# Kernel tuning notes

Measured on AMD Instinct MI355X. Metric: run time of the kernel, lower is better.

The kernel has to match this reference:

```python
import jax, jax.numpy as jnp
import numpy as np

NV, B, E, H, LF = 32, 32768, 16, 4, 4
D = E // H
FF = LF * E
EPS = 1e-5


def _gelu(x):
    return jax.nn.gelu(x, approximate=False)


def _ln(x, g, b):
    m = x.mean(-1, keepdims=True)
    v = ((x - m) ** 2).mean(-1, keepdims=True)
    return (x - m) * jax.lax.rsqrt(v + EPS) * g + b


def _mha(q_in, kv_in, wi, bi, wo, bo):
    # torch nn.MultiheadAttention, seq-first layout (S, B, E), eval mode (no dropout)
    wq, wk, wv = jnp.split(wi, 3, axis=0)
    bq, bk, bv = jnp.split(bi, 3)
    Sq, Bn = q_in.shape[0], q_in.shape[1]
    Sk = kv_in.shape[0]
    q = (q_in @ wq.T + bq).reshape(Sq, Bn, H, D)
    k = (kv_in @ wk.T + bk).reshape(Sk, Bn, H, D)
    v = (kv_in @ wv.T + bv).reshape(Sk, Bn, H, D)
    s = jnp.einsum('qbhd,kbhd->bhqk', q, k) / jnp.sqrt(jnp.asarray(D, q.dtype))
    a = jax.nn.softmax(s, axis=-1)
    o = jnp.einsum('bhqk,kbhd->qbhd', a, v).reshape(Sq, Bn, E)
    return o @ wo.T + bo


def setup_inputs() -> dict:
    key = jax.random.key(0)
    ks = iter(jax.random.split(key, 32))
    r = lambda *shape: 0.1 * jax.random.normal(next(ks), shape, dtype=jnp.float32)
    return {
        'x': jax.random.normal(next(ks), (B, NV), dtype=jnp.float32),
        'emb_w1': r(NV, LF), 'emb_b1': r(NV, LF),            # per-feature Linear(1, LF)
        'emb_w2': r(NV, LF, E), 'emb_b2': r(NV, E),          # per-feature Linear(LF, E)
        'ln1_g': jnp.ones((E,), jnp.float32), 'ln1_b': jnp.zeros((E,), jnp.float32),
        'attn_wi': r(3 * E, E), 'attn_bi': r(3 * E),
        'attn_wo': r(E, E), 'attn_bo': r(E),
        'ln2_g': jnp.ones((E,), jnp.float32), 'ln2_b': jnp.zeros((E,), jnp.float32),
        'fc1_w': r(FF, E), 'fc1_b': r(FF),
        'fc2_w': r(E, FF), 'fc2_b': r(E),
        'cls_token': jnp.zeros((E,), jnp.float32),
        'cln1_g': jnp.ones((E,), jnp.float32), 'cln1_b': jnp.zeros((E,), jnp.float32),
        'cattn_wi': r(3 * E, E), 'cattn_bi': r(3 * E),
        'cattn_wo': r(E, E), 'cattn_bo': r(E),
        'cln2_g': jnp.ones((E,), jnp.float32), 'cln2_b': jnp.zeros((E,), jnp.float32),
        'clsfc_w': r(1, E), 'clsfc_b': r(1),
    }


def reference(x, emb_w1, emb_b1, emb_w2, emb_b2, ln1_g, ln1_b,
              attn_wi, attn_bi, attn_wo, attn_bo, ln2_g, ln2_b,
              fc1_w, fc1_b, fc2_w, fc2_b, cls_token,
              cln1_g, cln1_b, cattn_wi, cattn_bi, cattn_wo, cattn_bo,
              cln2_g, cln2_b, clsfc_w, clsfc_b):
    # --- per-feature tokenizer: batched tiny MLPs (vectorized over nvars) ---
    h = _gelu(x[:, :, None] * emb_w1[None] + emb_b1[None])          # (B, NV, LF)
    e = _gelu(jnp.einsum('bvf,vfe->bve', h, emb_w2) + emb_b2[None]) # (B, NV, E)
    t = jnp.transpose(e, (1, 0, 2))                                 # (NV, B, E) seq-first
    # --- encoder block (pre-norm) ---
    res = t
    t = _ln(t, ln1_g, ln1_b)
    t = _mha(t, t, attn_wi, attn_bi, attn_wo, attn_bo) + res
    res = t
    t = _ln(t, ln2_g, ln2_b)
    t = _gelu(t @ fc1_w.T + fc1_b) @ fc2_w.T + fc2_b
    t = t + res
    # --- class-token decoder ---
    cls = jnp.broadcast_to(cls_token, (1, t.shape[1], E))           # (1, B, E)
    u = jnp.concatenate([cls, t], axis=0)                           # (NV+1, B, E)
    un = _ln(u, cln1_g, cln1_b)
    c = _mha(cls, un, cattn_wi, cattn_bi, cattn_wo, cattn_bo) + cls # query is raw cls
    c = _ln(c, cln2_g, cln2_b)
    c = c[0]                                                        # (B, E)
    out = jax.nn.sigmoid(c @ clsfc_w.T + clsfc_b)                   # (B, 1)
    return out
```

## Files before the change

### kernel.cpp

```cpp
#include <hip/hip_runtime.h>
#include <hip/hip_bf16.h>
#include <math.h>

#define NV 32
#define E  16
#define FF 64
#define BATCH 32768

static constexpr float EPS = 1e-5f;

typedef __attribute__((ext_vector_type(8)))  short bf16x8;
typedef __attribute__((ext_vector_type(16))) float f32x16;
typedef __attribute__((ext_vector_type(4)))  unsigned u32x4;

__device__ __forceinline__ short f2bf(float f) {
    __hip_bfloat16 h = __float2bfloat16(f);
    return __builtin_bit_cast(short, h);
}
__device__ __forceinline__ unsigned pack2(float a, float b) {
    return (unsigned)(unsigned short)f2bf(a) | ((unsigned)(unsigned short)f2bf(b) << 16);
}
__device__ __forceinline__ void halfswap(unsigned &a, unsigned &b, int hh) {
    const unsigned ax = (unsigned)__shfl_xor((int)a, 32);
    const unsigned bx = (unsigned)__shfl_xor((int)b, 32);
    const unsigned na = hh ? bx : a;
    const unsigned nb = hh ? b : ax;
    a = na; b = nb;
}
__device__ __forceinline__ int psi(int h, int i) {
    return 4 * h + (i & 3) + 8 * (i >> 2);
}
__device__ __forceinline__ float gelu_fast(float x) {
    const float x2 = x * x;
    const float u  = x * fmaf(x2, 0.07135481627f, 1.5957691216f);
    return x - x * __builtin_amdgcn_rcpf(1.0f + __expf(u));
}
__device__ __forceinline__ bf16x8 pack8(const float* v) {
    bf16x8 r;
#pragma unroll
    for (int i = 0; i < 8; i++) r[i] = f2bf(v[i]);
    return r;
}

__global__ __launch_bounds__(256, 4) void event_classifier_kernel(
    const float* __restrict__ x,
    const float* __restrict__ emb_w1,
    const float* __restrict__ emb_b1,
    const float* __restrict__ emb_w2,
    const float* __restrict__ emb_b2,
    const float* __restrict__ ln1_g, const float* __restrict__ ln1_b,
    const float* __restrict__ attn_wi,
    const float* __restrict__ attn_bi,
    const float* __restrict__ attn_wo,
    const float* __restrict__ attn_bo,
    const float* __restrict__ ln2_g, const float* __restrict__ ln2_b,
    const float* __restrict__ fc1_w,
    const float* __restrict__ fc1_b,
    const float* __restrict__ fc2_w,
    const float* __restrict__ fc2_b,
    const float* __restrict__ cls_token,
    const float* __restrict__ cln1_g, const float* __restrict__ cln1_b,
    const float* __restrict__ cattn_wi,
    const float* __restrict__ cattn_bi,
    const float* __restrict__ cattn_wo,
    const float* __restrict__ cattn_bo,
    const float* __restrict__ cln2_g, const float* __restrict__ cln2_b,
    const float* __restrict__ clsfc_w,
    const float* __restrict__ clsfc_b,
    float* __restrict__ out)
{
    __shared__ alignas(16) unsigned s_frag[13][64][4];
    __shared__ alignas(16) float s_bias[10][32];
    __shared__ alignas(16) unsigned short s_vt[4][4][5][40];
    __shared__ alignas(16) float s_cls[48];

    const int tid = threadIdx.x;
    const int l   = tid & 63;
    const int t   = l & 31;
    const int hh  = l >> 5;
    const int w   = tid >> 6;
    const int b   = blockIdx.x * 4 + w;

    for (int f0 = 0; f0 < 16; f0 += 4) {
        const int f = f0 + w;
        if (f < 13) {
            const float* W;
            switch (f) {
                case 0:  W = attn_wi;        break;
                case 1:  W = attn_wi + 256;  break;
                case 2:  W = attn_wi + 512;  break;
                case 3:  W = attn_wo;        break;
                case 4:  W = fc1_w;          break;
                case 5:  W = fc1_w + 512;    break;
                case 6: case 7: case 8: case 9: W = fc2_w; break;
                case 10: W = cattn_wi + 256; break;
                case 11: W = cattn_wi + 512; break;
                default: W = cattn_wo;       break;
            }
            const int stride = (f >= 6 && f <= 9) ? 64 : 16;
            const int coff   = (f >= 6 && f <= 9) ? (f - 6) * 16 : 0;
            const bool valid = (f == 4 || f == 5) ? true : (t < 16);
            const float scale = (f == 0) ? 0.5f : 1.0f;
            unsigned d0 = 0, d1 = 0, d2 = 0, d3 = 0;
            if (valid) {
                const float* row = W + t * stride + coff;
                d0 = pack2(row[psi(hh, 0)] * scale, row[psi(hh, 1)] * scale);
                d1 = pack2(row[psi(hh, 2)] * scale, row[psi(hh, 3)] * scale);
                d2 = pack2(row[psi(hh, 4)] * scale, row[psi(hh, 5)] * scale);
                d3 = pack2(row[psi(hh, 6)] * scale, row[psi(hh, 7)] * scale);
            }
            s_frag[f][l][0] = d0; s_frag[f][l][1] = d1;
            s_frag[f][l][2] = d2; s_frag[f][l][3] = d3;
        }
    }
    for (int i = tid; i < 10 * 32; i += 256) {
        const int mat = i >> 5, idx = i & 31, h2 = idx >> 4, r = idx & 15;
        const int p8 = psi(h2, r & 7);
        float val = 0.f;
        switch (mat) {
            case 0: if (r < 8) val = attn_bi[p8] * 0.5f; break;
            case 1: if (r < 8) val = attn_bi[16 + p8]; break;
            case 2: if (r < 8) val = attn_bi[32 + p8]; break;
            case 3: if (r < 8) val = attn_bo[p8]; break;
            case 4: val = fc1_b[psi(h2, r)]; break;
            case 5: val = fc1_b[32 + psi(h2, r)]; break;
            case 6: if (r < 8) val = fc2_b[p8]; break;
            case 7: if (r < 8) val = cattn_bi[16 + p8]; break;
            case 8: if (r < 8) val = cattn_bi[32 + p8]; break;
            default: if (r < 8) val = cattn_bo[p8] + cls_token[p8]; break;
        }
        s_bias[mat][idx] = val;
    }
    if (tid < 16) {
        const int jp = tid;
        float cls[E];
        float m = 0.f;
#pragma unroll
        for (int j = 0; j < E; j++) { cls[j] = cls_token[j]; m += cls[j]; }
        m *= (1.0f / E);
        float var = 0.f;
#pragma unroll
        for (int j = 0; j < E; j++) { float d = cls[j] - m; var += d * d; }
        var *= (1.0f / E);
        float r = rsqrtf(var + EPS);
        float un0[E];
#pragma unroll
        for (int j = 0; j < E; j++) un0[j] = (cls[j] - m) * r * cln1_g[j] + cln1_b[j];
        float qq = cattn_bi[jp], kk = cattn_bi[16 + jp], vv2 = cattn_bi[32 + jp];
#pragma unroll
        for (int j = 0; j < E; j++) {
            qq  += cls[j] * cattn_wi[jp * E + j];
            kk  += un0[j] * cattn_wi[(16 + jp) * E + j];
            vv2 += un0[j] * cattn_wi[(32 + jp) * E + j];
        }
        s_cls[jp] = qq * 0.5f; s_cls[16 + jp] = kk; s_cls[32 + jp] = vv2;
    }
    __syncthreads();

#define LD4(p) (*reinterpret_cast<const float4*>(p))
#define FRAG(f) (*reinterpret_cast<const bf16x8*>(&s_frag[f][l][0]))
#define CBIAS8(mat, c) { const float4 lo_ = LD4(&s_bias[mat][hh*16]); \
                         const float4 hi_ = LD4(&s_bias[mat][hh*16+4]); \
                         c[0]=lo_.x; c[1]=lo_.y; c[2]=lo_.z; c[3]=lo_.w; \
                         c[4]=hi_.x; c[5]=hi_.y; c[6]=hi_.z; c[7]=hi_.w; \
                         c[8]=0;c[9]=0;c[10]=0;c[11]=0;c[12]=0;c[13]=0;c[14]=0;c[15]=0; }
#define CBIAS16(mat, c) { const float4 a_ = LD4(&s_bias[mat][hh*16]); \
                          const float4 b_ = LD4(&s_bias[mat][hh*16+4]); \
                          const float4 c_ = LD4(&s_bias[mat][hh*16+8]); \
                          const float4 d_ = LD4(&s_bias[mat][hh*16+12]); \
                          c[0]=a_.x;c[1]=a_.y;c[2]=a_.z;c[3]=a_.w; \
                          c[4]=b_.x;c[5]=b_.y;c[6]=b_.z;c[7]=b_.w; \
                          c[8]=c_.x;c[9]=c_.y;c[10]=c_.z;c[11]=c_.w; \
                          c[12]=d_.x;c[13]=d_.y;c[14]=d_.z;c[15]=d_.w; }

    f32x16 z16;
#pragma unroll
    for (int i = 0; i < 16; i++) z16[i] = 0.0f;

    const float xv = x[b * NV + t];
    float F[8];
    {
        const float4 w1 = LD4(emb_w1 + t * 4);
        const float4 b1 = LD4(emb_b1 + t * 4);
        float hb[4];
        hb[0] = gelu_fast(fmaf(xv, w1.x, b1.x));
        hb[1] = gelu_fast(fmaf(xv, w1.y, b1.y));
        hb[2] = gelu_fast(fmaf(xv, w1.z, b1.z));
        hb[3] = gelu_fast(fmaf(xv, w1.w, b1.w));
        float a[8];
        const float4 bA = LD4(emb_b2 + t * 16 + 4 * hh);
        const float4 bB = LD4(emb_b2 + t * 16 + 8 + 4 * hh);
        a[0]=bA.x; a[1]=bA.y; a[2]=bA.z; a[3]=bA.w;
        a[4]=bB.x; a[5]=bB.y; a[6]=bB.z; a[7]=bB.w;
#pragma unroll
        for (int f = 0; f < 4; f++) {
            const float4 wA = LD4(emb_w2 + t * 64 + f * 16 + 4 * hh);
            const float4 wB = LD4(emb_w2 + t * 64 + f * 16 + 8 + 4 * hh);
            a[0] = fmaf(hb[f], wA.x, a[0]); a[1] = fmaf(hb[f], wA.y, a[1]);
            a[2] = fmaf(hb[f], wA.z, a[2]); a[3] = fmaf(hb[f], wA.w, a[3]);
            a[4] = fmaf(hb[f], wB.x, a[4]); a[5] = fmaf(hb[f], wB.y, a[5]);
            a[6] = fmaf(hb[f], wB.z, a[6]); a[7] = fmaf(hb[f], wB.w, a[7]);
        }
#pragma unroll
        for (int r = 0; r < 8; r++) F[r] = gelu_fast(a[r]);
    }

#define LN_CANON(gp, bp, src, dst) { \
        float s_ = 0.f; \
        _Pragma("unroll") for (int r = 0; r < 8; r++) s_ += src[r]; \
        s_ += __shfl_xor(s_, 32); \
        const float m_ = s_ * (1.0f / 16.0f); \
        float vs_ = 0.f; \
        _Pragma("unroll") for (int r = 0; r < 8; r++) { float d_ = src[r] - m_; vs_ += d_ * d_; } \
        vs_ += __shfl_xor(vs_, 32); \
        const float rs_ = rsqrtf(vs_ * (1.0f / 16.0f) + EPS); \
        const float4 gA_ = LD4(gp + 4 * hh), gB_ = LD4(gp + 8 + 4 * hh); \
        const float4 bA_ = LD4(bp + 4 * hh), bB_ = LD4(bp + 8 + 4 * hh); \
        dst[0] = (src[0]-m_)*rs_*gA_.x + bA_.x; dst[1] = (src[1]-m_)*rs_*gA_.y + bA_.y; \
        dst[2] = (src[2]-m_)*rs_*gA_.z + bA_.z; dst[3] = (src[3]-m_)*rs_*gA_.w + bA_.w; \
        dst[4] = (src[4]-m_)*rs_*gB_.x + bB_.x; dst[5] = (src[5]-m_)*rs_*gB_.y + bB_.y; \
        dst[6] = (src[6]-m_)*rs_*gB_.z + bB_.z; dst[7] = (src[7]-m_)*rs_*gB_.w + bB_.w; }

    float res[8];
#pragma unroll
    for (int r = 0; r < 8; r++) res[r] = F[r];
    float tn[8];
    LN_CANON(ln1_g, ln1_b, F, tn);

    const bf16x8 bt = pack8(tn);
    f32x16 cq, ck, cv;
    CBIAS8(0, cq); CBIAS8(1, ck); CBIAS8(2, cv);
    const f32x16 dq = __builtin_amdgcn_mfma_f32_32x32x16_bf16(FRAG(0), bt, cq, 0, 0, 0);
    const f32x16 dk = __builtin_amdgcn_mfma_f32_32x32x16_bf16(FRAG(1), bt, ck, 0, 0, 0);
    const f32x16 dv = __builtin_amdgcn_mfma_f32_32x32x16_bf16(FRAG(2), bt, cv, 0, 0, 0);

    unsigned qx0 = pack2(dq[0], dq[1]), qx1 = pack2(dq[2], dq[3]);
    unsigned qx2 = pack2(dq[4], dq[5]), qx3 = pack2(dq[6], dq[7]);
    unsigned kx0 = pack2(dk[0], dk[1]), kx1 = pack2(dk[2], dk[3]);
    unsigned kx2 = pack2(dk[4], dk[5]), kx3 = pack2(dk[6], dk[7]);
    halfswap(qx0, qx1, hh); halfswap(qx2, qx3, hh);
    halfswap(kx0, kx1, hh); halfswap(kx2, kx3, hh);

    s_vt[w][hh][0][t] = (unsigned short)f2bf(dv[0]);
    s_vt[w][hh][1][t] = (unsigned short)f2bf(dv[1]);
    s_vt[w][hh][2][t] = (unsigned short)f2bf(dv[2]);
    s_vt[w][hh][3][t] = (unsigned short)f2bf(dv[3]);
    s_vt[w][hh + 2][0][t] = (unsigned short)f2bf(dv[4]);
    s_vt[w][hh + 2][1][t] = (unsigned short)f2bf(dv[5]);
    s_vt[w][hh + 2][2][t] = (unsigned short)f2bf(dv[6]);
    s_vt[w][hh + 2][3][t] = (unsigned short)f2bf(dv[7]);
    s_vt[w][hh][4][t]     = 0x3F80;
    s_vt[w][hh + 2][4][t] = 0x3F80;
    asm volatile("s_waitcnt lgkmcnt(0)" ::: "memory");
    __builtin_amdgcn_sched_barrier(0);

    const int mr = (t < 5) ? t : 0;
    unsigned um0[4], um1[4];
#pragma unroll
    for (int h = 0; h < 4; h++) {
        const unsigned qf = (h == 0) ? qx0 : (h == 1) ? qx1 : (h == 2) ? qx2 : qx3;
        const unsigned kf = (h == 0) ? kx0 : (h == 1) ? kx1 : (h == 2) ? kx2 : kx3;
        const u32x4 au = {kf, 0u, 0u, 0u};
        const u32x4 bu = {qf, 0u, 0u, 0u};
        const f32x16 S = __builtin_amdgcn_mfma_f32_32x32x16_bf16(
            __builtin_bit_cast(bf16x8, au), __builtin_bit_cast(bf16x8, bu), z16, 0, 0, 0);
        unsigned w0 = pack2(__expf(S[0]),  __expf(S[1]));
        unsigned w1 = pack2(__expf(S[2]),  __expf(S[3]));
        unsigned w2 = pack2(__expf(S[4]),  __expf(S[5]));
        unsigned w3 = pack2(__expf(S[6]),  __expf(S[7]));
        unsigned w4 = pack2(__expf(S[8]),  __expf(S[9]));
        unsigned w5 = pack2(__expf(S[10]), __expf(S[11]));
        unsigned w6 = pack2(__expf(S[12]), __expf(S[13]));
        unsigned w7 = pack2(__expf(S[14]), __expf(S[15]));
        halfswap(w0, w2, hh); halfswap(w1, w3, hh);
        halfswap(w4, w6, hh); halfswap(w5, w7, hh);
        const u32x4 b1u = {w0, w1, w2, w3};
        const u32x4 b2u = {w4, w5, w6, w7};
        const bf16x8 A1 = *reinterpret_cast<const bf16x8*>(&s_vt[w][h][mr][8 * hh]);
        const bf16x8 A2 = *reinterpret_cast<const bf16x8*>(&s_vt[w][h][mr][8 * hh + 16]);
        f32x16 R = __builtin_amdgcn_mfma_f32_32x32x16_bf16(A1, __builtin_bit_cast(bf16x8, b1u), z16, 0, 0, 0);
        R = __builtin_amdgcn_mfma_f32_32x32x16_bf16(A2, __builtin_bit_cast(bf16x8, b2u), R, 0, 0, 0);
        const float Lv = __shfl_xor(R[0], 32);
        const float rl = __builtin_amdgcn_rcpf(hh ? 1.0f : Lv);
        um0[h] = pack2(R[0] * rl, R[1] * rl);
        um1[h] = pack2(R[2] * rl, R[3] * rl);
    }
    halfswap(um0[0], um0[1], hh); halfswap(um1[0], um1[1], hh);
    halfswap(um0[2], um0[3], hh); halfswap(um1[2], um1[3], hh);
    const u32x4 bou = {um0[0], um1[0], um0[2], um1[2]};
    const bf16x8 bo = __builtin_bit_cast(bf16x8, bou);

    {
        f32x16 co; CBIAS8(3, co);
        const f32x16 dto = __builtin_amdgcn_mfma_f32_32x32x16_bf16(FRAG(3), bo, co, 0, 0, 0);
#pragma unroll
        for (int r = 0; r < 8; r++) F[r] = dto[r] + res[r];
    }

#pragma unroll
    for (int r = 0; r < 8; r++) res[r] = F[r];
    float tn2[8];
    LN_CANON(ln2_g, ln2_b, F, tn2);
    {
        const bf16x8 bt2 = pack8(tn2);
        f32x16 c1, c2;
        CBIAS16(4, c1); CBIAS16(5, c2);
        const f32x16 g1 = __builtin_amdgcn_mfma_f32_32x32x16_bf16(FRAG(4), bt2, c1, 0, 0, 0);
        const f32x16 g2 = __builtin_amdgcn_mfma_f32_32x32x16_bf16(FRAG(5), bt2, c2, 0, 0, 0);
        float gva[16], gvb[16];
#pragma unroll
        for (int r = 0; r < 16; r++) gva[r] = gelu_fast(g1[r]);
#pragma unroll
        for (int r = 0; r < 16; r++) gvb[r] = gelu_fast(g2[r]);
        const bf16x8 pk0 = pack8(gva), pk1 = pack8(gva + 8);
        const bf16x8 pk2 = pack8(gvb), pk3 = pack8(gvb + 8);
        f32x16 acc; CBIAS8(6, acc);
        acc = __builtin_amdgcn_mfma_f32_32x32x16_bf16(FRAG(6), pk0, acc, 0, 0, 0);
        acc = __builtin_amdgcn_mfma_f32_32x32x16_bf16(FRAG(7), pk1, acc, 0, 0, 0);
        acc = __builtin_amdgcn_mfma_f32_32x32x16_bf16(FRAG(8), pk2, acc, 0, 0, 0);
        acc = __builtin_amdgcn_mfma_f32_32x32x16_bf16(FRAG(9), pk3, acc, 0, 0, 0);
#pragma unroll
        for (int r = 0; r < 8; r++) F[r] = acc[r] + res[r];
    }

    float tn3[8];
    LN_CANON(cln1_g, cln1_b, F, tn3);
    const bf16x8 bt3 = pack8(tn3);
    f32x16 ckc, cvc;
    CBIAS8(7, ckc); CBIAS8(8, cvc);
    const f32x16 dkc = __builtin_amdgcn_mfma_f32_32x32x16_bf16(FRAG(10), bt3, ckc, 0, 0, 0);
    const f32x16 dvc = __builtin_amdgcn_mfma_f32_32x32x16_bf16(FRAG(11), bt3, cvc, 0, 0, 0);

    const float4 qcA = LD4(s_cls + 4 * hh);
    const float4 qcB = LD4(s_cls + 8 + 4 * hh);
    const float sA2 = fmaf(qcA.x, dkc[0], fmaf(qcA.y, dkc[1], fmaf(qcA.z, dkc[2], qcA.w * dkc[3])));
    const float sB2 = fmaf(qcB.x, dkc[4], fmaf(qcB.y, dkc[5], fmaf(qcB.z, dkc[6], qcB.w * dkc[7])));
    const float pA2 = __expf(sA2), pB2 = __expf(sB2);
    const float4 k0A = LD4(s_cls + 16 + 4 * hh);
    const float4 k0B = LD4(s_cls + 16 + 8 + 4 * hh);
    const float s0A = fmaf(qcA.x, k0A.x, fmaf(qcA.y, k0A.y, fmaf(qcA.z, k0A.z, qcA.w * k0A.w)));
    const float s0B = fmaf(qcB.x, k0B.x, fmaf(qcB.y, k0B.y, fmaf(qcB.z, k0B.z, qcB.w * k0B.w)));
    const float p0A = __expf(s0A), p0B = __expf(s0B);

    float lA2 = pA2, lB2 = pB2;
    float oc[8];
    oc[0] = pA2 * dvc[0]; oc[1] = pA2 * dvc[1]; oc[2] = pA2 * dvc[2]; oc[3] = pA2 * dvc[3];
    oc[4] = pB2 * dvc[4]; oc[5] = pB2 * dvc[5]; oc[6] = pB2 * dvc[6]; oc[7] = pB2 * dvc[7];
#pragma unroll
    for (int mask = 1; mask <= 16; mask <<= 1) {
        lA2 += __shfl_xor(lA2, mask);
        lB2 += __shfl_xor(lB2, mask);
#pragma unroll
        for (int r = 0; r < 8; r++) oc[r] += __shfl_xor(oc[r], mask);
    }
    {
        const float4 v0A = LD4(s_cls + 32 + 4 * hh);
        const float4 v0B = LD4(s_cls + 32 + 8 + 4 * hh);
        const float rA2 = __builtin_amdgcn_rcpf(lA2 + p0A);
        const float rB2 = __builtin_amdgcn_rcpf(lB2 + p0B);
        oc[0] = (oc[0] + p0A * v0A.x) * rA2; oc[1] = (oc[1] + p0A * v0A.y) * rA2;
        oc[2] = (oc[2] + p0A * v0A.z) * rA2; oc[3] = (oc[3] + p0A * v0A.w) * rA2;
        oc[4] = (oc[4] + p0B * v0B.x) * rB2; oc[5] = (oc[5] + p0B * v0B.y) * rB2;
        oc[6] = (oc[6] + p0B * v0B.z) * rB2; oc[7] = (oc[7] + p0B * v0B.w) * rB2;
    }

    float c8[8];
    {
        const bf16x8 boc = pack8(oc);
        f32x16 cc; CBIAS8(9, cc);
        const f32x16 dc = __builtin_amdgcn_mfma_f32_32x32x16_bf16(FRAG(12), boc, cc, 0, 0, 0);
#pragma unroll
        for (int r = 0; r < 8; r++) c8[r] = dc[r];
    }
    {
        float s = 0.f;
#pragma unroll
        for (int r = 0; r < 8; r++) s += c8[r];
        s += __shfl_xor(s, 32);
        const float m = s * (1.0f / 16.0f);
        float vs = 0.f;
#pragma unroll
        for (int r = 0; r < 8; r++) { const float d = c8[r] - m; vs += d * d; }
        vs += __shfl_xor(vs, 32);
        const float rstd = rsqrtf(vs * (1.0f / 16.0f) + EPS);
        const float4 gA = LD4(cln2_g + 4 * hh), gB = LD4(cln2_g + 8 + 4 * hh);
        const float4 bA = LD4(cln2_b + 4 * hh), bB = LD4(cln2_b + 8 + 4 * hh);
        const float4 wA = LD4(clsfc_w + 4 * hh), wB = LD4(clsfc_w + 8 + 4 * hh);
        float zp = 0.f;
        zp = fmaf((c8[0]-m)*rstd*gA.x + bA.x, wA.x, zp);
        zp = fmaf((c8[1]-m)*rstd*gA.y + bA.y, wA.y, zp);
        zp = fmaf((c8[2]-m)*rstd*gA.z + bA.z, wA.z, zp);
        zp = fmaf((c8[3]-m)*rstd*gA.w + bA.w, wA.w, zp);
        zp = fmaf((c8[4]-m)*rstd*gB.x + bB.x, wB.x, zp);
        zp = fmaf((c8[5]-m)*rstd*gB.y + bB.y, wB.y, zp);
        zp = fmaf((c8[6]-m)*rstd*gB.z + bB.z, wB.z, zp);
        zp = fmaf((c8[7]-m)*rstd*gB.w + bB.w, wB.w, zp);
        const float z = zp + __shfl_xor(zp, 32) + clsfc_b[0];
        const float sig = __builtin_amdgcn_rcpf(1.0f + __expf(-z));
        if (l == 0) out[b] = sig;
    }
}

extern "C" void kernel_launch(void* const* d_in, const int* in_sizes, int n_in,
                              void* d_out, int out_size, void* d_ws, size_t ws_size,
                              hipStream_t stream) {
    const float* x        = (const float*)d_in[0];
    const float* emb_w1   = (const float*)d_in[1];
    const float* emb_b1   = (const float*)d_in[2];
    const float* emb_w2   = (const float*)d_in[3];
    const float* emb_b2   = (const float*)d_in[4];
    const float* ln1_g    = (const float*)d_in[5];
    const float* ln1_b    = (const float*)d_in[6];
    const float* attn_wi  = (const float*)d_in[7];
    const float* attn_bi  = (const float*)d_in[8];
    const float* attn_wo  = (const float*)d_in[9];
    const float* attn_bo  = (const float*)d_in[10];
    const float* ln2_g    = (const float*)d_in[11];
    const float* ln2_b    = (const float*)d_in[12];
    const float* fc1_w    = (const float*)d_in[13];
    const float* fc1_b    = (const float*)d_in[14];
    const float* fc2_w    = (const float*)d_in[15];
    const float* fc2_b    = (const float*)d_in[16];
    const float* cls_tok  = (const float*)d_in[17];
    const float* cln1_g   = (const float*)d_in[18];
    const float* cln1_b   = (const float*)d_in[19];
    const float* cattn_wi = (const float*)d_in[20];
    const float* cattn_bi = (const float*)d_in[21];
    const float* cattn_wo = (const float*)d_in[22];
    const float* cattn_bo = (const float*)d_in[23];
    const float* cln2_g   = (const float*)d_in[24];
    const float* cln2_b   = (const float*)d_in[25];
    const float* clsfc_w  = (const float*)d_in[26];
    const float* clsfc_b  = (const float*)d_in[27];
    float* out = (float*)d_out;

    const int grid = BATCH / 4;
    event_classifier_kernel<<<grid, 256, 0, stream>>>(
        x, emb_w1, emb_b1, emb_w2, emb_b2, ln1_g, ln1_b,
        attn_wi, attn_bi, attn_wo, attn_bo, ln2_g, ln2_b,
        fc1_w, fc1_b, fc2_w, fc2_b, cls_tok,
        cln1_g, cln1_b, cattn_wi, cattn_bi, cattn_wo, cattn_bo,
        cln2_g, cln2_b, clsfc_w, clsfc_b, out);
}
```

Before: 106.9 us.

## Fold layernorm affine into weights, merge QK/KV MFMAs, use permlane32 swaps and exp2

Folds the LayerNorm gamma/beta into the following projection weights and biases, so the per-token normalisation drops its affine step. Q and K are packed into one 32-row MFMA, and the decoder's K and V likewise, cutting the MFMA count. Cross-half shuffles are replaced with permlane32_swap, and softmax/GELU/sigmoid exponentials use exp2 with log2(e) pre-folded into scales. The final LN2-gain times classifier weights is precomputed in shared memory. This changes bf16 rounding points, because the gains are now folded into the bf16 weights.

```diff
diff --git a/kernel.cpp b/kernel.cpp
--- a/kernel.cpp
+++ b/kernel.cpp
@@ -6,6 +6,7 @@
 #define E  16
 #define FF 64
 #define BATCH 32768
+#define L2E 1.4426950408889634f
 
 static constexpr float EPS = 1e-5f;
 
@@ -20,26 +21,35 @@
 __device__ __forceinline__ unsigned pack2(float a, float b) {
     return (unsigned)(unsigned short)f2bf(a) | ((unsigned)(unsigned short)f2bf(b) << 16);
 }
-__device__ __forceinline__ void halfswap(unsigned &a, unsigned &b, int hh) {
-    const unsigned ax = (unsigned)__shfl_xor((int)a, 32);
-    const unsigned bx = (unsigned)__shfl_xor((int)b, 32);
-    const unsigned na = hh ? bx : a;
-    const unsigned nb = hh ? b : ax;
-    a = na; b = nb;
+__device__ __forceinline__ void halfswap(unsigned &a, unsigned &b) {
+    const auto r = __builtin_amdgcn_permlane32_swap(a, b, false, false);
+    a = (unsigned)r[0]; b = (unsigned)r[1];
+}
+__device__ __forceinline__ float addxhalf(float v) {
+    const unsigned u = __builtin_bit_cast(unsigned, v);
+    const auto r = __builtin_amdgcn_permlane32_swap(u, u, false, false);
+    return __builtin_bit_cast(float, (unsigned)r[0]) + __builtin_bit_cast(float, (unsigned)r[1]);
 }
 __device__ __forceinline__ int psi(int h, int i) {
     return 4 * h + (i & 3) + 8 * (i >> 2);
 }
+__device__ __forceinline__ float ex2(float x) { return __builtin_amdgcn_exp2f(x); }
 __device__ __forceinline__ float gelu_fast(float x) {
     const float x2 = x * x;
-    const float u  = x * fmaf(x2, 0.07135481627f, 1.5957691216f);
-    return x - x * __builtin_amdgcn_rcpf(1.0f + __expf(u));
+    const float u  = x * fmaf(x2, 0.10294324f, 2.3022082f);
+    return x - x * __builtin_amdgcn_rcpf(1.0f + ex2(u));
 }
 __device__ __forceinline__ bf16x8 pack8(const float* v) {
     bf16x8 r;
 #pragma unroll
     for (int i = 0; i < 8; i++) r[i] = f2bf(v[i]);
     return r;
+}
+__device__ __forceinline__ float dot16(const float* __restrict__ wrow, const float* __restrict__ v) {
+    float s = 0.f;
+#pragma unroll
+    for (int j = 0; j < 16; j++) s = fmaf(wrow[j], v[j], s);
+    return s;
 }
 
 __global__ __launch_bounds__(256, 4) void event_classifier_kernel(
@@ -69,10 +79,11 @@
     const float* __restrict__ clsfc_b,
     float* __restrict__ out)
 {
-    __shared__ alignas(16) unsigned s_frag[13][64][4];
-    __shared__ alignas(16) float s_bias[10][32];
+    __shared__ alignas(16) unsigned s_frag[11][64][4];
+    __shared__ alignas(16) float s_bias[8][32];
     __shared__ alignas(16) unsigned short s_vt[4][4][5][40];
     __shared__ alignas(16) float s_cls[48];
+    __shared__ alignas(16) float s_cw[20];
 
     const int tid = threadIdx.x;
     const int l   = tid & 63;
@@ -81,52 +92,56 @@
     const int w   = tid >> 6;
     const int b   = blockIdx.x * 4 + w;
 
-    for (int f0 = 0; f0 < 16; f0 += 4) {
+    for (int f0 = 0; f0 < 12; f0 += 4) {
         const int f = f0 + w;
-        if (f < 13) {
-            const float* W;
+        if (f < 11) {
+            const float* W; const float* gc = nullptr;
+            int stride = 16, coff = 0; bool valid = true; float rscale = 1.0f;
             switch (f) {
-                case 0:  W = attn_wi;        break;
-                case 1:  W = attn_wi + 256;  break;
-                case 2:  W = attn_wi + 512;  break;
-                case 3:  W = attn_wo;        break;
-                case 4:  W = fc1_w;          break;
-                case 5:  W = fc1_w + 512;    break;
-                case 6: case 7: case 8: case 9: W = fc2_w; break;
-                case 10: W = cattn_wi + 256; break;
-                case 11: W = cattn_wi + 512; break;
-                default: W = cattn_wo;       break;
+                case 0:  W = attn_wi;        gc = ln1_g; if (t < 16) rscale = 0.5f * L2E; break;
+                case 1:  W = attn_wi + 512;  gc = ln1_g; valid = (t < 16); break;
+                case 2:  W = attn_wo;        valid = (t < 16); break;
+                case 3:  W = fc1_w;          gc = ln2_g; break;
+                case 4:  W = fc1_w + 512;    gc = ln2_g; break;
+                case 5: case 6: case 7: case 8:
+                         W = fc2_w; stride = 64; coff = (f - 5) * 16; valid = (t < 16); break;
+                case 9:  W = cattn_wi + 256; gc = cln1_g; break;
+                default: W = cattn_wo;       valid = (t < 16); break;
             }
-            const int stride = (f >= 6 && f <= 9) ? 64 : 16;
-            const int coff   = (f >= 6 && f <= 9) ? (f - 6) * 16 : 0;
-            const bool valid = (f == 4 || f == 5) ? true : (t < 16);
-            const float scale = (f == 0) ? 0.5f : 1.0f;
-            unsigned d0 = 0, d1 = 0, d2 = 0, d3 = 0;
+            unsigned d[4] = {0u, 0u, 0u, 0u};
             if (valid) {
                 const float* row = W + t * stride + coff;
-                d0 = pack2(row[psi(hh, 0)] * scale, row[psi(hh, 1)] * scale);
-                d1 = pack2(row[psi(hh, 2)] * scale, row[psi(hh, 3)] * scale);
-                d2 = pack2(row[psi(hh, 4)] * scale, row[psi(hh, 5)] * scale);
-                d3 = pack2(row[psi(hh, 6)] * scale, row[psi(hh, 7)] * scale);
+#pragma unroll
+                for (int e2 = 0; e2 < 4; e2++) {
+                    const int p0 = psi(hh, 2 * e2), p1 = psi(hh, 2 * e2 + 1);
+                    const float g0 = gc ? gc[p0] : 1.0f;
+                    const float g1 = gc ? gc[p1] : 1.0f;
+                    d[e2] = pack2(row[p0] * g0 * rscale, row[p1] * g1 * rscale);
+                }
             }
-            s_frag[f][l][0] = d0; s_frag[f][l][1] = d1;
-            s_frag[f][l][2] = d2; s_frag[f][l][3] = d3;
+            s_frag[f][l][0] = d[0]; s_frag[f][l][1] = d[1];
+            s_frag[f][l][2] = d[2]; s_frag[f][l][3] = d[3];
         }
     }
-    for (int i = tid; i < 10 * 32; i += 256) {
+    {
+        const int i = tid;
         const int mat = i >> 5, idx = i & 31, h2 = idx >> 4, r = idx & 15;
         const int p8 = psi(h2, r & 7);
         float val = 0.f;
         switch (mat) {
-            case 0: if (r < 8) val = attn_bi[p8] * 0.5f; break;
-            case 1: if (r < 8) val = attn_bi[16 + p8]; break;
-            case 2: if (r < 8) val = attn_bi[32 + p8]; break;
-            case 3: if (r < 8) val = attn_bo[p8]; break;
-            case 4: val = fc1_b[psi(h2, r)]; break;
-            case 5: val = fc1_b[32 + psi(h2, r)]; break;
-            case 6: if (r < 8) val = fc2_b[p8]; break;
-            case 7: if (r < 8) val = cattn_bi[16 + p8]; break;
-            case 8: if (r < 8) val = cattn_bi[32 + p8]; break;
+            case 0:
+                if (r < 8) val = (attn_bi[p8] + dot16(attn_wi + p8 * 16, ln1_b)) * (0.5f * L2E);
+                else       val =  attn_bi[16 + p8] + dot16(attn_wi + (16 + p8) * 16, ln1_b);
+                break;
+            case 1: if (r < 8) val = attn_bi[32 + p8] + dot16(attn_wi + (32 + p8) * 16, ln1_b); break;
+            case 2: if (r < 8) val = attn_bo[p8]; break;
+            case 3: { const int p16 = psi(h2, r); val = fc1_b[p16] + dot16(fc1_w + p16 * 16, ln2_b); } break;
+            case 4: { const int p16 = psi(h2, r); val = fc1_b[32 + p16] + dot16(fc1_w + (32 + p16) * 16, ln2_b); } break;
+            case 5: if (r < 8) val = fc2_b[p8]; break;
+            case 6:
+                if (r < 8) val = cattn_bi[16 + p8] + dot16(cattn_wi + (16 + p8) * 16, cln1_b);
+                else       val = cattn_bi[32 + p8] + dot16(cattn_wi + (32 + p8) * 16, cln1_b);
+                break;
             default: if (r < 8) val = cattn_bo[p8] + cls_token[p8]; break;
         }
         s_bias[mat][idx] = val;
@@ -153,7 +168,14 @@
             kk  += un0[j] * cattn_wi[(16 + jp) * E + j];
             vv2 += un0[j] * cattn_wi[(32 + jp) * E + j];
         }
-        s_cls[jp] = qq * 0.5f; s_cls[16 + jp] = kk; s_cls[32 + jp] = vv2;
+        s_cls[jp] = qq * (0.5f * L2E); s_cls[16 + jp] = kk; s_cls[32 + jp] = vv2;
+        s_cw[jp] = cln2_g[jp] * clsfc_w[jp];
+        if (jp == 0) {
+            float s = clsfc_b[0];
+#pragma unroll
+            for (int j = 0; j < E; j++) s = fmaf(cln2_b[j], clsfc_w[j], s);
+            s_cw[16] = s;
+        }
     }
     __syncthreads();
 
@@ -205,41 +227,35 @@
         for (int r = 0; r < 8; r++) F[r] = gelu_fast(a[r]);
     }
 
-#define LN_CANON(gp, bp, src, dst) { \
+#define LN_CANON(src, dst) { \
         float s_ = 0.f; \
         _Pragma("unroll") for (int r = 0; r < 8; r++) s_ += src[r]; \
-        s_ += __shfl_xor(s_, 32); \
+        s_ = addxhalf(s_); \
         const float m_ = s_ * (1.0f / 16.0f); \
         float vs_ = 0.f; \
-        _Pragma("unroll") for (int r = 0; r < 8; r++) { float d_ = src[r] - m_; vs_ += d_ * d_; } \
-        vs_ += __shfl_xor(vs_, 32); \
+        _Pragma("unroll") for (int r = 0; r < 8; r++) { float d_ = src[r] - m_; vs_ = fmaf(d_, d_, vs_); } \
+        vs_ = addxhalf(vs_); \
         const float rs_ = rsqrtf(vs_ * (1.0f / 16.0f) + EPS); \
-        const float4 gA_ = LD4(gp + 4 * hh), gB_ = LD4(gp + 8 + 4 * hh); \
-        const float4 bA_ = LD4(bp + 4 * hh), bB_ = LD4(bp + 8 + 4 * hh); \
-        dst[0] = (src[0]-m_)*rs_*gA_.x + bA_.x; dst[1] = (src[1]-m_)*rs_*gA_.y + bA_.y; \
-        dst[2] = (src[2]-m_)*rs_*gA_.z + bA_.z; dst[3] = (src[3]-m_)*rs_*gA_.w + bA_.w; \
-        dst[4] = (src[4]-m_)*rs_*gB_.x + bB_.x; dst[5] = (src[5]-m_)*rs_*gB_.y + bB_.y; \
-        dst[6] = (src[6]-m_)*rs_*gB_.z + bB_.z; dst[7] = (src[7]-m_)*rs_*gB_.w + bB_.w; }
+        _Pragma("unroll") for (int r = 0; r < 8; r++) dst[r] = (src[r] - m_) * rs_; }
 
     float res[8];
 #pragma unroll
     for (int r = 0; r < 8; r++) res[r] = F[r];
     float tn[8];
-    LN_CANON(ln1_g, ln1_b, F, tn);
+    LN_CANON(F, tn);
 
     const bf16x8 bt = pack8(tn);
-    f32x16 cq, ck, cv;
-    CBIAS8(0, cq); CBIAS8(1, ck); CBIAS8(2, cv);
-    const f32x16 dq = __builtin_amdgcn_mfma_f32_32x32x16_bf16(FRAG(0), bt, cq, 0, 0, 0);
-    const f32x16 dk = __builtin_amdgcn_mfma_f32_32x32x16_bf16(FRAG(1), bt, ck, 0, 0, 0);
-    const f32x16 dv = __builtin_amdgcn_mfma_f32_32x32x16_bf16(FRAG(2), bt, cv, 0, 0, 0);
-
-    unsigned qx0 = pack2(dq[0], dq[1]), qx1 = pack2(dq[2], dq[3]);
-    unsigned qx2 = pack2(dq[4], dq[5]), qx3 = pack2(dq[6], dq[7]);
-    unsigned kx0 = pack2(dk[0], dk[1]), kx1 = pack2(dk[2], dk[3]);
-    unsigned kx2 = pack2(dk[4], dk[5]), kx3 = pack2(dk[6], dk[7]);
-    halfswap(qx0, qx1, hh); halfswap(qx2, qx3, hh);
-    halfswap(kx0, kx1, hh); halfswap(kx2, kx3, hh);
+    f32x16 cqk, cv;
+    CBIAS16(0, cqk); CBIAS8(1, cv);
+    const f32x16 dqk = __builtin_amdgcn_mfma_f32_32x32x16_bf16(FRAG(0), bt, cqk, 0, 0, 0);
+    const f32x16 dv  = __builtin_amdgcn_mfma_f32_32x32x16_bf16(FRAG(1), bt, cv, 0, 0, 0);
+
+    unsigned qx0 = pack2(dqk[0],  dqk[1]),  qx1 = pack2(dqk[2],  dqk[3]);
+    unsigned qx2 = pack2(dqk[4],  dqk[5]),  qx3 = pack2(dqk[6],  dqk[7]);
+    unsigned kx0 = pack2(dqk[8],  dqk[9]),  kx1 = pack2(dqk[10], dqk[11]);
+    unsigned kx2 = pack2(dqk[12], dqk[13]), kx3 = pack2(dqk[14], dqk[15]);
+    halfswap(qx0, qx1); halfswap(qx2, qx3);
+    halfswap(kx0, kx1); halfswap(kx2, kx3);
 
     s_vt[w][hh][0][t] = (unsigned short)f2bf(dv[0]);
     s_vt[w][hh][1][t] = (unsigned short)f2bf(dv[1]);
@@ -264,35 +280,36 @@
         const u32x4 bu = {qf, 0u, 0u, 0u};
         const f32x16 S = __builtin_amdgcn_mfma_f32_32x32x16_bf16(
             __builtin_bit_cast(bf16x8, au), __builtin_bit_cast(bf16x8, bu), z16, 0, 0, 0);
-        unsigned w0 = pack2(__expf(S[0]),  __expf(S[1]));
-        unsigned w1 = pack2(__expf(S[2]),  __expf(S[3]));
-        unsigned w2 = pack2(__expf(S[4]),  __expf(S[5]));
-        unsigned w3 = pack2(__expf(S[6]),  __expf(S[7]));
-        unsigned w4 = pack2(__expf(S[8]),  __expf(S[9]));
-        unsigned w5 = pack2(__expf(S[10]), __expf(S[11]));
-        unsigned w6 = pack2(__expf(S[12]), __expf(S[13]));
-        unsigned w7 = pack2(__expf(S[14]), __expf(S[15]));
-        halfswap(w0, w2, hh); halfswap(w1, w3, hh);
-        halfswap(w4, w6, hh); halfswap(w5, w7, hh);
+        unsigned w0 = pack2(ex2(S[0]),  ex2(S[1]));
+        unsigned w1 = pack2(ex2(S[2]),  ex2(S[3]));
+        unsigned w2 = pack2(ex2(S[4]),  ex2(S[5]));
+        unsigned w3 = pack2(ex2(S[6]),  ex2(S[7]));
+        unsigned w4 = pack2(ex2(S[8]),  ex2(S[9]));
+        unsigned w5 = pack2(ex2(S[10]), ex2(S[11]));
+        unsigned w6 = pack2(ex2(S[12]), ex2(S[13]));
+        unsigned w7 = pack2(ex2(S[14]), ex2(S[15]));
+        halfswap(w0, w2); halfswap(w1, w3);
+        halfswap(w4, w6); halfswap(w5, w7);
         const u32x4 b1u = {w0, w1, w2, w3};
         const u32x4 b2u = {w4, w5, w6, w7};
         const bf16x8 A1 = *reinterpret_cast<const bf16x8*>(&s_vt[w][h][mr][8 * hh]);
         const bf16x8 A2 = *reinterpret_cast<const bf16x8*>(&s_vt[w][h][mr][8 * hh + 16]);
         f32x16 R = __builtin_amdgcn_mfma_f32_32x32x16_bf16(A1, __builtin_bit_cast(bf16x8, b1u), z16, 0, 0, 0);
         R = __builtin_amdgcn_mfma_f32_32x32x16_bf16(A2, __builtin_bit_cast(bf16x8, b2u), R, 0, 0, 0);
-        const float Lv = __shfl_xor(R[0], 32);
-        const float rl = __builtin_amdgcn_rcpf(hh ? 1.0f : Lv);
+        const unsigned ru = __builtin_bit_cast(unsigned, R[0]);
+        const auto rr = __builtin_amdgcn_permlane32_swap(ru, ru, false, false);
+        const float rl = __builtin_amdgcn_rcpf(__builtin_bit_cast(float, (unsigned)rr[1]));
         um0[h] = pack2(R[0] * rl, R[1] * rl);
         um1[h] = pack2(R[2] * rl, R[3] * rl);
     }
-    halfswap(um0[0], um0[1], hh); halfswap(um1[0], um1[1], hh);
-    halfswap(um0[2], um0[3], hh); halfswap(um1[2], um1[3], hh);
+    halfswap(um0[0], um0[1]); halfswap(um1[0], um1[1]);
+    halfswap(um0[2], um0[3]); halfswap(um1[2], um1[3]);
     const u32x4 bou = {um0[0], um1[0], um0[2], um1[2]};
     const bf16x8 bo = __builtin_bit_cast(bf16x8, bou);
 
     {
-        f32x16 co; CBIAS8(3, co);
-        const f32x16 dto = __builtin_amdgcn_mfma_f32_32x32x16_bf16(FRAG(3), bo, co, 0, 0, 0);
+        f32x16 co; CBIAS8(2, co);
+        const f32x16 dto = __builtin_amdgcn_mfma_f32_32x32x16_bf16(FRAG(2), bo, co, 0, 0, 0);
 #pragma unroll
         for (int r = 0; r < 8; r++) F[r] = dto[r] + res[r];
     }
@@ -300,13 +317,13 @@
 #pragma unroll
     for (int r = 0; r < 8; r++) res[r] = F[r];
     float tn2[8];
-    LN_CANON(ln2_g, ln2_b, F, tn2);
+    LN_CANON(F, tn2);
     {
         const bf16x8 bt2 = pack8(tn2);
         f32x16 c1, c2;
-        CBIAS16(4, c1); CBIAS16(5, c2);
-        const f32x16 g1 = __builtin_amdgcn_mfma_f32_32x32x16_bf16(FRAG(4), bt2, c1, 0, 0, 0);
-        const f32x16 g2 = __builtin_amdgcn_mfma_f32_32x32x16_bf16(FRAG(5), bt2, c2, 0, 0, 0);
+        CBIAS16(3, c1); CBIAS16(4, c2);
+        const f32x16 g1 = __builtin_amdgcn_mfma_f32_32x32x16_bf16(FRAG(3), bt2, c1, 0, 0, 0);
+        const f32x16 g2 = __builtin_amdgcn_mfma_f32_32x32x16_bf16(FRAG(4), bt2, c2, 0, 0, 0);
         float gva[16], gvb[16];
 #pragma unroll
         for (int r = 0; r < 16; r++) gva[r] = gelu_fast(g1[r]);
@@ -314,38 +331,36 @@
         for (int r = 0; r < 16; r++) gvb[r] = gelu_fast(g2[r]);
         const bf16x8 pk0 = pack8(gva), pk1 = pack8(gva + 8);
         const bf16x8 pk2 = pack8(gvb), pk3 = pack8(gvb + 8);
-        f32x16 acc; CBIAS8(6, acc);
-        acc = __builtin_amdgcn_mfma_f32_32x32x16_bf16(FRAG(6), pk0, acc, 0, 0, 0);
-        acc = __builtin_amdgcn_mfma_f32_32x32x16_bf16(FRAG(7), pk1, acc, 0, 0, 0);
-        acc = __builtin_amdgcn_mfma_f32_32x32x16_bf16(FRAG(8), pk2, acc, 0, 0, 0);
-        acc = __builtin_amdgcn_mfma_f32_32x32x16_bf16(FRAG(9), pk3, acc, 0, 0, 0);
+        f32x16 acc; CBIAS8(5, acc);
+        acc = __builtin_amdgcn_mfma_f32_32x32x16_bf16(FRAG(5), pk0, acc, 0, 0, 0);
+        acc = __builtin_amdgcn_mfma_f32_32x32x16_bf16(FRAG(6), pk1, acc, 0, 0, 0);
+        acc = __builtin_amdgcn_mfma_f32_32x32x16_bf16(FRAG(7), pk2, acc, 0, 0, 0);
+        acc = __builtin_amdgcn_mfma_f32_32x32x16_bf16(FRAG(8), pk3, acc, 0, 0, 0);
 #pragma unroll
         for (int r = 0; r < 8; r++) F[r] = acc[r] + res[r];
     }
 
     float tn3[8];
-    LN_CANON(cln1_g, cln1_b, F, tn3);
+    LN_CANON(F, tn3);
     const bf16x8 bt3 = pack8(tn3);
-    f32x16 ckc, cvc;
-    CBIAS8(7, ckc); CBIAS8(8, cvc);
-    const f32x16 dkc = __builtin_amdgcn_mfma_f32_32x32x16_bf16(FRAG(10), bt3, ckc, 0, 0, 0);
-    const f32x16 dvc = __builtin_amdgcn_mfma_f32_32x32x16_bf16(FRAG(11), bt3, cvc, 0, 0, 0);
+    f32x16 ckv; CBIAS16(6, ckv);
+    const f32x16 dkv = __builtin_amdgcn_mfma_f32_32x32x16_bf16(FRAG(9), bt3, ckv, 0, 0, 0);
 
     const float4 qcA = LD4(s_cls + 4 * hh);
     const float4 qcB = LD4(s_cls + 8 + 4 * hh);
-    const float sA2 = fmaf(qcA.x, dkc[0], fmaf(qcA.y, dkc[1], fmaf(qcA.z, dkc[2], qcA.w * dkc[3])));
-    const float sB2 = fmaf(qcB.x, dkc[4], fmaf(qcB.y, dkc[5], fmaf(qcB.z, dkc[6], qcB.w * dkc[7])));
-    const float pA2 = __expf(sA2), pB2 = __expf(sB2);
+    const float sA2 = fmaf(qcA.x, dkv[0], fmaf(qcA.y, dkv[1], fmaf(qcA.z, dkv[2], qcA.w * dkv[3])));
+    const float sB2 = fmaf(qcB.x, dkv[4], fmaf(qcB.y, dkv[5], fmaf(qcB.z, dkv[6], qcB.w * dkv[7])));
+    const float pA2 = ex2(sA2), pB2 = ex2(sB2);
     const float4 k0A = LD4(s_cls + 16 + 4 * hh);
     const float4 k0B = LD4(s_cls + 16 + 8 + 4 * hh);
     const float s0A = fmaf(qcA.x, k0A.x, fmaf(qcA.y, k0A.y, fmaf(qcA.z, k0A.z, qcA.w * k0A.w)));
     const float s0B = fmaf(qcB.x, k0B.x, fmaf(qcB.y, k0B.y, fmaf(qcB.z, k0B.z, qcB.w * k0B.w)));
-    const float p0A = __expf(s0A), p0B = __expf(s0B);
+    const float p0A = ex2(s0A), p0B = ex2(s0B);
 
     float lA2 = pA2, lB2 = pB2;
     float oc[8];
-    oc[0] = pA2 * dvc[0]; oc[1] = pA2 * dvc[1]; oc[2] = pA2 * dvc[2]; oc[3] = pA2 * dvc[3];
-    oc[4] = pB2 * dvc[4]; oc[5] = pB2 * dvc[5]; oc[6] = pB2 * dvc[6]; oc[7] = pB2 * dvc[7];
+    oc[0] = pA2 * dkv[8];  oc[1] = pA2 * dkv[9];  oc[2] = pA2 * dkv[10]; oc[3] = pA2 * dkv[11];
+    oc[4] = pB2 * dkv[12]; oc[5] = pB2 * dkv[13]; oc[6] = pB2 * dkv[14]; oc[7] = pB2 * dkv[15];
 #pragma unroll
     for (int mask = 1; mask <= 16; mask <<= 1) {
         lA2 += __shfl_xor(lA2, mask);
@@ -367,8 +382,8 @@
     float c8[8];
     {
         const bf16x8 boc = pack8(oc);
-        f32x16 cc; CBIAS8(9, cc);
-        const f32x16 dc = __builtin_amdgcn_mfma_f32_32x32x16_bf16(FRAG(12), boc, cc, 0, 0, 0);
+        f32x16 cc; CBIAS8(7, cc);
+        const f32x16 dc = __builtin_amdgcn_mfma_f32_32x32x16_bf16(FRAG(10), boc, cc, 0, 0, 0);
 #pragma unroll
         for (int r = 0; r < 8; r++) c8[r] = dc[r];
     }
@@ -376,27 +391,25 @@
         float s = 0.f;
 #pragma unroll
         for (int r = 0; r < 8; r++) s += c8[r];
-        s += __shfl_xor(s, 32);
+        s = addxhalf(s);
         const float m = s * (1.0f / 16.0f);
         float vs = 0.f;
 #pragma unroll
-        for (int r = 0; r < 8; r++) { const float d = c8[r] - m; vs += d * d; }
-        vs += __shfl_xor(vs, 32);
+        for (int r = 0; r < 8; r++) { const float d = c8[r] - m; vs = fmaf(d, d, vs); }
+        vs = addxhalf(vs);
         const float rstd = rsqrtf(vs * (1.0f / 16.0f) + EPS);
-        const float4 gA = LD4(cln2_g + 4 * hh), gB = LD4(cln2_g + 8 + 4 * hh);
-        const float4 bA = LD4(cln2_b + 4 * hh), bB = LD4(cln2_b + 8 + 4 * hh);
-        const float4 wA = LD4(clsfc_w + 4 * hh), wB = LD4(clsfc_w + 8 + 4 * hh);
+        const float4 wA = LD4(s_cw + 4 * hh), wB = LD4(s_cw + 8 + 4 * hh);
         float zp = 0.f;
-        zp = fmaf((c8[0]-m)*rstd*gA.x + bA.x, wA.x, zp);
-        zp = fmaf((c8[1]-m)*rstd*gA.y + bA.y, wA.y, zp);
-        zp = fmaf((c8[2]-m)*rstd*gA.z + bA.z, wA.z, zp);
-        zp = fmaf((c8[3]-m)*rstd*gA.w + bA.w, wA.w, zp);
-        zp = fmaf((c8[4]-m)*rstd*gB.x + bB.x, wB.x, zp);
-        zp = fmaf((c8[5]-m)*rstd*gB.y + bB.y, wB.y, zp);
-        zp = fmaf((c8[6]-m)*rstd*gB.z + bB.z, wB.z, zp);
-        zp = fmaf((c8[7]-m)*rstd*gB.w + bB.w, wB.w, zp);
-        const float z = zp + __shfl_xor(zp, 32) + clsfc_b[0];
-        const float sig = __builtin_amdgcn_rcpf(1.0f + __expf(-z));
+        zp = fmaf((c8[0] - m) * rstd, wA.x, zp);
+        zp = fmaf((c8[1] - m) * rstd, wA.y, zp);
+        zp = fmaf((c8[2] - m) * rstd, wA.z, zp);
+        zp = fmaf((c8[3] - m) * rstd, wA.w, zp);
+        zp = fmaf((c8[4] - m) * rstd, wB.x, zp);
+        zp = fmaf((c8[5] - m) * rstd, wB.y, zp);
+        zp = fmaf((c8[6] - m) * rstd, wB.z, zp);
+        zp = fmaf((c8[7] - m) * rstd, wB.w, zp);
+        const float z = addxhalf(zp) + s_cw[16];
+        const float sig = __builtin_amdgcn_rcpf(1.0f + ex2(-L2E * z));
         if (l == 0) out[b] = sig;
     }
 }
```

Result: faster. 97.04 us (-9.2%).
